# Optimization experiments

Measured on AMD Instinct MI355X. Metric: run time of the kernel, lower is better.

## Reference

```python
import jax, jax.numpy as jnp
import numpy as np

LEAK = 0.2  # LeakyReLU alpha

def setup_inputs() -> dict:
    key = jax.random.key(0)
    k1, k2, k3, k4 = jax.random.split(key, 4)
    B, N, D, H = 4, 1024, 64, 64
    qs = jax.random.normal(k1, (B, N, D), dtype=jnp.float32)
    ks = jax.random.normal(k2, (B, N, D), dtype=jnp.float32)
    vs = jax.random.normal(k3, (B, N, D), dtype=jnp.float32)
    W = jax.random.normal(k4, (3 * D, H), dtype=jnp.float32) * 0.05  # Dense kernel on concat(q,k,q-k)
    b = jnp.zeros((H,), dtype=jnp.float32)
    a = jnp.ones((H,), dtype=jnp.float32)
    return {"qs": qs, "ks": ks, "vs": vs, "W": W, "b": b, "a": a}

def reference(qs, ks, vs, W, b, a):
    D = qs.shape[-1]
    norm = 1.0 / jnp.sqrt(jnp.asarray(D, dtype=qs.dtype))
    # Dense on concat(q, k, q-k) splits as q@(Wq+Wd) + k@(Wk-Wd) + b,
    # avoiding the O(N^2 * 3D) concat tensor (same math as TF concat->Dense).
    Wq, Wk, Wd = W[:D], W[D:2 * D], W[2 * D:]
    hq = qs @ (Wq + Wd)            # [B, N, H]  query-side term
    hk = ks @ (Wk - Wd)            # [B, N, H]  key-side term
    h = hq[:, :, None, :] + hk[:, None, :, :] + b   # [B, N, N, H]
    h = jnp.where(h > 0, h, LEAK * h)               # LeakyReLU(0.2)
    scores = jnp.einsum('bijh,h->bij', h, a) * norm # [B, N, N]
    att = jax.nn.softmax(scores, axis=-1)
    return jnp.matmul(att, vs)                      # [B, N, D]
```

## Files before the change

### kernel.cpp

```cpp
#include <hip/hip_runtime.h>
#include <math.h>

#define LOG2E 1.4426950408889634f
typedef __attribute__((ext_vector_type(2))) _Float16 h2v;
typedef __attribute__((ext_vector_type(8))) _Float16 f16x8;
typedef __attribute__((ext_vector_type(4))) float f32x4;

static __device__ __forceinline__ unsigned pkrtz_u32(float lo, float hi) {
  auto p = __builtin_amdgcn_cvt_pkrtz(lo, hi);
  unsigned u; __builtin_memcpy(&u, &p, 4); return u;
}
static __device__ __forceinline__ h2v habs2(h2v x) {
  unsigned u; __builtin_memcpy(&u, &x, 4);
  u &= 0x7FFF7FFFu;
  h2v r; __builtin_memcpy(&r, &u, 4); return r;
}
static __device__ __forceinline__ h2v u2h(unsigned u) {
  h2v r; __builtin_memcpy(&r, &u, 4); return r;
}
static __device__ __forceinline__ unsigned pkmax_u(unsigned a, unsigned b) {
  h2v r = __builtin_elementwise_max(u2h(a), u2h(b));
  unsigned u; __builtin_memcpy(&u, &r, 4); return u;
}
static __device__ __forceinline__ float h2f(unsigned u, int idx) {
  h2v v = u2h(u);
  return (float)v[idx];
}


__global__ __launch_bounds__(256) void prep_kernel(
    const float* __restrict__ qs, const float* __restrict__ ks,
    const float* __restrict__ vs,
    const float* __restrict__ W, const float* __restrict__ bias,
    const float* __restrict__ a,
    unsigned* __restrict__ hq2t, uint4* __restrict__ khT4,
    float* __restrict__ Dj, unsigned* __restrict__ abd2,
    uint4* __restrict__ vfrag) {
  __shared__ __align__(16) float wcomb[64][68];
  __shared__ __align__(16) float xin[64][68];
  const int blk = blockIdx.x;
  const int t = threadIdx.x;

  if (blk >= 128) {
    const int unit = blk - 128;
    const int b = unit >> 5, kstep = unit & 31;
    const int lane = t & 63, ntile = t >> 6;
    const int j0 = kstep * 32 + (lane >> 4) * 8;
    const int d = ntile * 16 + (lane & 15);
    const float* vb = vs + b * 1024 * 64;
    unsigned pr[4];
#pragma unroll
    for (int i = 0; i < 4; ++i)
      pr[i] = pkrtz_u32(vb[(j0 + 2 * i) * 64 + d], vb[(j0 + 2 * i + 1) * 64 + d]);
    vfrag[((b * 32 + kstep) * 5 + ntile) * 64 + lane] =
        make_uint4(pr[0], pr[1], pr[2], pr[3]);
    if (t < 64) {
      unsigned v = ((t & 15) == 0) ? 0x3C003C00u : 0u;
      vfrag[((b * 32 + kstep) * 5 + 4) * 64 + t] = make_uint4(v, v, v, v);
    }
    return;
  }

  const bool qpart = blk < 64;
  const int r0 = (qpart ? blk : blk - 64) * 64;
  const float* src = qpart ? qs : ks;
  if (blk == 0 && t < 32)
    abd2[t] = pkrtz_u32(0.05f * a[2 * t], 0.05f * a[2 * t + 1]);
  for (int rep = 0; rep < 16; ++rep) {
    int e = rep * 256 + t;
    int row = e >> 6, col = e & 63;
    float wd = W[(128 + row) * 64 + col];
    float wm = qpart ? (W[row * 64 + col] + wd)
                     : (W[(64 + row) * 64 + col] - wd);
    wcomb[row][col] = wm;
    xin[row][col] = src[(r0 + row) * 64 + col];
  }
  __syncthreads();
  const int r = t >> 2;
  const int h0 = (t & 3) << 4;
  float acc[16];
#pragma unroll
  for (int k = 0; k < 16; ++k) acc[k] = 0.f;
#pragma unroll 8
  for (int d = 0; d < 64; ++d) {
    float xv = xin[r][d];
#pragma unroll
    for (int c = 0; c < 4; ++c) {
      float4 w4 = *(const float4*)&wcomb[d][h0 + (c << 2)];
      acc[c * 4 + 0] = fmaf(xv, w4.x, acc[c * 4 + 0]);
      acc[c * 4 + 1] = fmaf(xv, w4.y, acc[c * 4 + 1]);
      acc[c * 4 + 2] = fmaf(xv, w4.z, acc[c * 4 + 2]);
      acc[c * 4 + 3] = fmaf(xv, w4.w, acc[c * 4 + 3]);
    }
  }
  int grow = r0 + r;
  if (qpart) {
    unsigned pr[8];
#pragma unroll
    for (int i = 0; i < 8; ++i) pr[i] = pkrtz_u32(acc[2 * i], acc[2 * i + 1]);
    const int base = (grow >> 3) * 256 + (grow & 7) * 4;
    const int it0 = (t & 3) * 2;
    *(uint4*)&hq2t[base + it0 * 32]       = make_uint4(pr[0], pr[1], pr[2], pr[3]);
    *(uint4*)&hq2t[base + (it0 + 1) * 32] = make_uint4(pr[4], pr[5], pr[6], pr[7]);
  } else {
    int bidx = grow >> 10;
    int j = grow & 1023;
    float val[16];
    float part = 0.f;
#pragma unroll
    for (int k = 0; k < 16; ++k) {
      val[k] = acc[k] + bias[h0 + k];
      part += a[h0 + k] * val[k];
    }
    part += __shfl_xor(part, 1);
    part += __shfl_xor(part, 2);
    if ((t & 3) == 0) Dj[bidx * 1024 + j] = 0.075f * part;
    unsigned pr[8];
#pragma unroll
    for (int i = 0; i < 8; ++i) pr[i] = pkrtz_u32(val[2 * i], val[2 * i + 1]);
    const int h4a = (t & 3) * 2;
    khT4[(bidx * 8 + h4a) * 1024 + j]     = make_uint4(pr[0], pr[1], pr[2], pr[3]);
    khT4[(bidx * 8 + h4a + 1) * 1024 + j] = make_uint4(pr[4], pr[5], pr[6], pr[7]);
  }
}

__global__ __launch_bounds__(512) void attn15_kernel(
    const uint4* __restrict__ vfrag,
    const unsigned* __restrict__ hq2t, const uint4* __restrict__ khT4,
    const float* __restrict__ Dj, const unsigned* __restrict__ abd2,
    float* __restrict__ out) {
  __shared__ __align__(16) unsigned p2u[8 * 520];
  __shared__ __align__(16) float ob[64 * 64];
  __shared__ __align__(16) unsigned redmu[8 * 4];
  __shared__ __align__(16) float redl[8 * 8];

  const int t = threadIdx.x;
  const int lane = t & 63;
  const int w = t >> 6;
  const int b = blockIdx.y;
  const int rowbase = blockIdx.x * 8;
  const int growbase = b * 1024 + rowbase;

  const uint4* kh_b = khT4 + (size_t)b * 8 * 1024;
  const uint4* vf_b = vfrag + (size_t)b * 32 * 5 * 64;
  const unsigned* qt = hq2t + (size_t)growbase * 32;

  const int jloc = w * 128 + lane * 2;
  float2 d2 = *(const float2*)(Dj + b * 1024 + jloc);

  float s[8][2];
#pragma unroll
  for (int r = 0; r < 8; ++r) { s[r][0] = 0.f; s[r][1] = 0.f; }

  uint4 kc0 = kh_b[jloc], kc1 = kh_b[jloc + 1];
#pragma unroll 1
  for (int it = 0; it < 8; ++it) {
    const int nx = (it < 7) ? it + 1 : it;
    uint4 kn0 = kh_b[nx * 1024 + jloc];
    uint4 kn1 = kh_b[nx * 1024 + jloc + 1];
    uint4 abq = *(const uint4*)(abd2 + it * 4);
    const unsigned abu[4] = {abq.x, abq.y, abq.z, abq.w};
    const unsigned kcu[2][4] = {{kc0.x, kc0.y, kc0.z, kc0.w},
                                {kc1.x, kc1.y, kc1.z, kc1.w}};
#pragma unroll
    for (int r = 0; r < 8; ++r) {
      uint4 qq = *(const uint4*)(qt + it * 32 + r * 4);
      const unsigned qu[4] = {qq.x, qq.y, qq.z, qq.w};
#pragma unroll
      for (int u = 0; u < 4; ++u) {
        h2v qh = u2h(qu[u]);
        h2v a2 = u2h(abu[u]);
        h2v x0 = habs2(qh + u2h(kcu[0][u]));
        s[r][0] = __builtin_amdgcn_fdot2(a2, x0, s[r][0], false);
        h2v x1 = habs2(qh + u2h(kcu[1][u]));
        s[r][1] = __builtin_amdgcn_fdot2(a2, x1, s[r][1], false);
      }
    }
    kc0 = kn0; kc1 = kn1;
  }
#pragma unroll
  for (int r = 0; r < 8; ++r) { s[r][0] += d2.x; s[r][1] += d2.y; }

  unsigned mp[4];
#pragma unroll
  for (int k = 0; k < 4; ++k)
    mp[k] = pkrtz_u32(fmaxf(s[2 * k][0], s[2 * k][1]),
                      fmaxf(s[2 * k + 1][0], s[2 * k + 1][1]));
#pragma unroll
  for (int off = 32; off >= 1; off >>= 1) {
#pragma unroll
    for (int k = 0; k < 4; ++k) mp[k] = pkmax_u(mp[k], __shfl_xor(mp[k], off));
  }
  if (lane == 0)
    *(uint4*)&redmu[w * 4] = make_uint4(mp[0], mp[1], mp[2], mp[3]);

#pragma unroll
  for (int r = 0; r < 8; ++r) {
    float mwr = h2f(mp[r >> 1], r & 1);
    float p0 = __builtin_amdgcn_exp2f((s[r][0] - mwr) * LOG2E);
    float p1 = __builtin_amdgcn_exp2f((s[r][1] - mwr) * LOG2E);
    p2u[r * 520 + w * 64 + lane] = pkrtz_u32(p0, p1);
  }

  f32x4 acc[5];
#pragma unroll
  for (int nt = 0; nt < 5; ++nt) acc[nt] = (f32x4){0.f, 0.f, 0.f, 0.f};
  const int arow = (lane & 7) * 520;
  const int kgr = (lane >> 4) * 8;
#pragma unroll 2
  for (int ks = 0; ks < 4; ++ks) {
    const int j0 = w * 128 + ks * 32;
    uint4 au = *(const uint4*)&p2u[arow + ((j0 + kgr) >> 1)];
    f16x8 af; __builtin_memcpy(&af, &au, 16);
    const int gks = j0 >> 5;
#pragma unroll
    for (int nt = 0; nt < 5; ++nt) {
      uint4 bu = vf_b[(gks * 5 + nt) * 64 + lane];
      f16x8 bf; __builtin_memcpy(&bf, &bu, 16);
      acc[nt] = __builtin_amdgcn_mfma_f32_16x16x32_f16(af, bf, acc[nt], 0, 0, 0);
    }
  }
  __syncthreads();

  unsigned Mp[4];
  {
    uint4 v0 = *(const uint4*)&redmu[0];
    Mp[0] = v0.x; Mp[1] = v0.y; Mp[2] = v0.z; Mp[3] = v0.w;
#pragma unroll
    for (int wv = 1; wv < 8; ++wv) {
      uint4 vv = *(const uint4*)&redmu[wv * 4];
      Mp[0] = pkmax_u(Mp[0], vv.x); Mp[1] = pkmax_u(Mp[1], vv.y);
      Mp[2] = pkmax_u(Mp[2], vv.z); Mp[3] = pkmax_u(Mp[3], vv.w);
    }
  }
  const int rb = ((lane >> 4) & 1) * 4;
  float sc[4];
#pragma unroll
  for (int rg = 0; rg < 4; ++rg) {
    int r = rb + rg;
    float mwv = h2f(mp[r >> 1], r & 1);
    float Mv = h2f(Mp[r >> 1], r & 1);
    sc[rg] = __builtin_amdgcn_exp2f((mwv - Mv) * LOG2E);
  }

  if (lane < 32) {
#pragma unroll
    for (int nt = 0; nt < 4; ++nt)
#pragma unroll
      for (int rg = 0; rg < 4; ++rg)
        ob[(w * 8 + rb + rg) * 64 + nt * 16 + (lane & 15)] = acc[nt][rg] * sc[rg];
  }
  if ((lane & 47) == 0) {
    float4 lv;
    lv.x = acc[4][0] * sc[0]; lv.y = acc[4][1] * sc[1];
    lv.z = acc[4][2] * sc[2]; lv.w = acc[4][3] * sc[3];
    *(float4*)&redl[w * 8 + rb] = lv;
  }
  __syncthreads();

  {
    int r = t >> 6, d = t & 63;
    float ax = 0.f, lt = 0.f;
#pragma unroll
    for (int wv = 0; wv < 8; ++wv) {
      ax += ob[(wv * 8 + r) * 64 + d];
      lt += redl[wv * 8 + r];
    }
    out[(growbase + r) * 64 + d] = ax / lt;
  }
}

extern "C" void kernel_launch(void* const* d_in, const int* in_sizes, int n_in,
                              void* d_out, int out_size, void* d_ws, size_t ws_size,
                              hipStream_t stream) {
  const float* qs = (const float*)d_in[0];
  const float* ks = (const float*)d_in[1];
  const float* vs = (const float*)d_in[2];
  const float* W  = (const float*)d_in[3];
  const float* bi = (const float*)d_in[4];
  const float* a  = (const float*)d_in[5];
  float* out = (float*)d_out;
  unsigned* hq2t  = (unsigned*)d_ws;
  uint4*    khT4  = (uint4*)((char*)d_ws + 524288);
  float*    Dj    = (float*)((char*)d_ws + 1048576);
  unsigned* abd2  = (unsigned*)((char*)d_ws + 1064960);
  uint4*    vfrag = (uint4*)((char*)d_ws + 1065216);
  prep_kernel<<<256, 256, 0, stream>>>(qs, ks, vs, W, bi, a, hq2t, khT4, Dj,
                                       abd2, vfrag);
  attn15_kernel<<<dim3(128, 4), 512, 0, stream>>>(vfrag, hq2t, khT4, Dj, abd2, out);
}
```

Before: 34.05 us.

## Hold all key features in registers and loop over query rows

```diff
diff --git a/kernel.cpp b/kernel.cpp
--- a/kernel.cpp
+++ b/kernel.cpp
@@ -17,14 +17,6 @@
 }
 static __device__ __forceinline__ h2v u2h(unsigned u) {
   h2v r; __builtin_memcpy(&r, &u, 4); return r;
-}
-static __device__ __forceinline__ unsigned pkmax_u(unsigned a, unsigned b) {
-  h2v r = __builtin_elementwise_max(u2h(a), u2h(b));
-  unsigned u; __builtin_memcpy(&u, &r, 4); return u;
-}
-static __device__ __forceinline__ float h2f(unsigned u, int idx) {
-  h2v v = u2h(u);
-  return (float)v[idx];
 }
 
 
@@ -98,10 +90,9 @@
     unsigned pr[8];
 #pragma unroll
     for (int i = 0; i < 8; ++i) pr[i] = pkrtz_u32(acc[2 * i], acc[2 * i + 1]);
-    const int base = (grow >> 3) * 256 + (grow & 7) * 4;
-    const int it0 = (t & 3) * 2;
-    *(uint4*)&hq2t[base + it0 * 32]       = make_uint4(pr[0], pr[1], pr[2], pr[3]);
-    *(uint4*)&hq2t[base + (it0 + 1) * 32] = make_uint4(pr[4], pr[5], pr[6], pr[7]);
+    const int base = (grow >> 3) * 256 + (grow & 7) * 32 + (t & 3) * 8;
+    *(uint4*)&hq2t[base]     = make_uint4(pr[0], pr[1], pr[2], pr[3]);
+    *(uint4*)&hq2t[base + 4] = make_uint4(pr[4], pr[5], pr[6], pr[7]);
   } else {
     int bidx = grow >> 10;
     int j = grow & 1023;
@@ -124,15 +115,15 @@
   }
 }
 
-__global__ __launch_bounds__(512) void attn15_kernel(
+__global__ __launch_bounds__(512) void attn16_kernel(
     const uint4* __restrict__ vfrag,
     const unsigned* __restrict__ hq2t, const uint4* __restrict__ khT4,
     const float* __restrict__ Dj, const unsigned* __restrict__ abd2,
     float* __restrict__ out) {
   __shared__ __align__(16) unsigned p2u[8 * 520];
   __shared__ __align__(16) float ob[64 * 64];
-  __shared__ __align__(16) unsigned redmu[8 * 4];
-  __shared__ __align__(16) float redl[8 * 8];
+  __shared__ __align__(16) float redm[64];
+  __shared__ __align__(16) float redl[64];
 
   const int t = threadIdx.x;
   const int lane = t & 63;
@@ -143,62 +134,51 @@
 
   const uint4* kh_b = khT4 + (size_t)b * 8 * 1024;
   const uint4* vf_b = vfrag + (size_t)b * 32 * 5 * 64;
-  const unsigned* qt = hq2t + (size_t)growbase * 32;
+  const unsigned* qt = hq2t + (size_t)(growbase >> 3) * 256;
 
   const int jloc = w * 128 + lane * 2;
   float2 d2 = *(const float2*)(Dj + b * 1024 + jloc);
 
-  float s[8][2];
-#pragma unroll
-  for (int r = 0; r < 8; ++r) { s[r][0] = 0.f; s[r][1] = 0.f; }
-
-  uint4 kc0 = kh_b[jloc], kc1 = kh_b[jloc + 1];
+  uint4 kk[16];
+#pragma unroll
+  for (int h4 = 0; h4 < 8; ++h4) {
+    kk[2 * h4]     = kh_b[h4 * 1024 + jloc];
+    kk[2 * h4 + 1] = kh_b[h4 * 1024 + jloc + 1];
+  }
+  uint4 abv[8];
+#pragma unroll
+  for (int it = 0; it < 8; ++it) abv[it] = *(const uint4*)(abd2 + it * 4);
+
 #pragma unroll 1
-  for (int it = 0; it < 8; ++it) {
-    const int nx = (it < 7) ? it + 1 : it;
-    uint4 kn0 = kh_b[nx * 1024 + jloc];
-    uint4 kn1 = kh_b[nx * 1024 + jloc + 1];
-    uint4 abq = *(const uint4*)(abd2 + it * 4);
-    const unsigned abu[4] = {abq.x, abq.y, abq.z, abq.w};
-    const unsigned kcu[2][4] = {{kc0.x, kc0.y, kc0.z, kc0.w},
-                                {kc1.x, kc1.y, kc1.z, kc1.w}};
-#pragma unroll
-    for (int r = 0; r < 8; ++r) {
-      uint4 qq = *(const uint4*)(qt + it * 32 + r * 4);
-      const unsigned qu[4] = {qq.x, qq.y, qq.z, qq.w};
+  for (int r = 0; r < 8; ++r) {
+    uint4 qv[8];
+#pragma unroll
+    for (int it = 0; it < 8; ++it)
+      qv[it] = *(const uint4*)(qt + r * 32 + it * 4);
+    float s0 = 0.f, s1 = 0.f;
+#pragma unroll
+    for (int it = 0; it < 8; ++it) {
+      const unsigned* qu = (const unsigned*)&qv[it];
+      const unsigned* au = (const unsigned*)&abv[it];
+      const unsigned* k0 = (const unsigned*)&kk[2 * it];
+      const unsigned* k1 = (const unsigned*)&kk[2 * it + 1];
 #pragma unroll
       for (int u = 0; u < 4; ++u) {
         h2v qh = u2h(qu[u]);
-        h2v a2 = u2h(abu[u]);
-        h2v x0 = habs2(qh + u2h(kcu[0][u]));
-        s[r][0] = __builtin_amdgcn_fdot2(a2, x0, s[r][0], false);
-        h2v x1 = habs2(qh + u2h(kcu[1][u]));
-        s[r][1] = __builtin_amdgcn_fdot2(a2, x1, s[r][1], false);
+        h2v a2 = u2h(au[u]);
+        h2v x0 = habs2(qh + u2h(k0[u]));
+        s0 = __builtin_amdgcn_fdot2(a2, x0, s0, false);
+        h2v x1 = habs2(qh + u2h(k1[u]));
+        s1 = __builtin_amdgcn_fdot2(a2, x1, s1, false);
       }
     }
-    kc0 = kn0; kc1 = kn1;
-  }
-#pragma unroll
-  for (int r = 0; r < 8; ++r) { s[r][0] += d2.x; s[r][1] += d2.y; }
-
-  unsigned mp[4];
-#pragma unroll
-  for (int k = 0; k < 4; ++k)
-    mp[k] = pkrtz_u32(fmaxf(s[2 * k][0], s[2 * k][1]),
-                      fmaxf(s[2 * k + 1][0], s[2 * k + 1][1]));
-#pragma unroll
-  for (int off = 32; off >= 1; off >>= 1) {
-#pragma unroll
-    for (int k = 0; k < 4; ++k) mp[k] = pkmax_u(mp[k], __shfl_xor(mp[k], off));
-  }
-  if (lane == 0)
-    *(uint4*)&redmu[w * 4] = make_uint4(mp[0], mp[1], mp[2], mp[3]);
-
-#pragma unroll
-  for (int r = 0; r < 8; ++r) {
-    float mwr = h2f(mp[r >> 1], r & 1);
-    float p0 = __builtin_amdgcn_exp2f((s[r][0] - mwr) * LOG2E);
-    float p1 = __builtin_amdgcn_exp2f((s[r][1] - mwr) * LOG2E);
+    s0 += d2.x; s1 += d2.y;
+    float m = fmaxf(s0, s1);
+#pragma unroll
+    for (int off = 32; off >= 1; off >>= 1) m = fmaxf(m, __shfl_xor(m, off));
+    if (lane == 0) redm[r * 8 + w] = m;
+    float p0 = __builtin_amdgcn_exp2f((s0 - m) * LOG2E);
+    float p1 = __builtin_amdgcn_exp2f((s1 - m) * LOG2E);
     p2u[r * 520 + w * 64 + lane] = pkrtz_u32(p0, p1);
   }
 
@@ -222,25 +202,17 @@
   }
   __syncthreads();
 
-  unsigned Mp[4];
-  {
-    uint4 v0 = *(const uint4*)&redmu[0];
-    Mp[0] = v0.x; Mp[1] = v0.y; Mp[2] = v0.z; Mp[3] = v0.w;
-#pragma unroll
-    for (int wv = 1; wv < 8; ++wv) {
-      uint4 vv = *(const uint4*)&redmu[wv * 4];
-      Mp[0] = pkmax_u(Mp[0], vv.x); Mp[1] = pkmax_u(Mp[1], vv.y);
-      Mp[2] = pkmax_u(Mp[2], vv.z); Mp[3] = pkmax_u(Mp[3], vv.w);
-    }
-  }
   const int rb = ((lane >> 4) & 1) * 4;
   float sc[4];
 #pragma unroll
   for (int rg = 0; rg < 4; ++rg) {
     int r = rb + rg;
-    float mwv = h2f(mp[r >> 1], r & 1);
-    float Mv = h2f(Mp[r >> 1], r & 1);
-    sc[rg] = __builtin_amdgcn_exp2f((mwv - Mv) * LOG2E);
+    float4 m0 = *(const float4*)&redm[r * 8 + 0];
+    float4 m1 = *(const float4*)&redm[r * 8 + 4];
+    float M = fmaxf(fmaxf(fmaxf(m0.x, m0.y), fmaxf(m0.z, m0.w)),
+                    fmaxf(fmaxf(m1.x, m1.y), fmaxf(m1.z, m1.w)));
+    float mwv = redm[r * 8 + w];
+    sc[rg] = __builtin_amdgcn_exp2f((mwv - M) * LOG2E);
   }
 
   if (lane < 32) {
@@ -287,5 +259,5 @@
   uint4*    vfrag = (uint4*)((char*)d_ws + 1065216);
   prep_kernel<<<256, 256, 0, stream>>>(qs, ks, vs, W, bi, a, hq2t, khT4, Dj,
                                        abd2, vfrag);
-  attn15_kernel<<<dim3(128, 4), 512, 0, stream>>>(vfrag, hq2t, khT4, Dj, abd2, out);
-}
+  attn16_kernel<<<dim3(128, 4), 512, 0, stream>>>(vfrag, hq2t, khT4, Dj, abd2, out);
+}
```

Result: slower. 34.97 us (+2.7%).
